# Kernel tuning notes

Hardware: AMD Instinct MI355X
Metric: run time of the kernel (lower is better)

Reference implementation:

```python
import jax, jax.numpy as jnp
import numpy as np

HEADS = 2
DIM_HEAD = 1
HIDDEN = HEADS * DIM_HEAD
SCALE = DIM_HEAD ** (-0.5)


def setup_inputs() -> dict:
    key = jax.random.key(0)
    ks = jax.random.split(key, 5)
    B, C, H, W, Z = 2, 64, 128, 128, 16
    return {
        "x": jax.random.normal(ks[0], (B, C, H, W, Z), dtype=jnp.float32),
        "query": jax.random.normal(ks[1], (B, C, H, W, Z), dtype=jnp.float32),
        "W_qkv": jax.random.normal(ks[2], (3 * HIDDEN, C), dtype=jnp.float32) * 0.1,
        "W_q": jax.random.normal(ks[3], (HIDDEN, C), dtype=jnp.float32) * 0.1,
        "W_out": jax.random.normal(ks[4], (C, HIDDEN), dtype=jnp.float32) * 0.1,
        "b_out": jnp.zeros((C,), dtype=jnp.float32),
    }


def reference(x, query, W_qkv, W_q, W_out, b_out):
    b, c, h, w, z = x.shape
    n = h * w * z
    xf = x.reshape(b, c, n)          # [b, c, n]
    qf = query.reshape(b, query.shape[1], n)

    # 1x1 conv3d == per-voxel linear projection; q-chunk of to_qkv is discarded
    k = jnp.einsum('bcn,oc->bon', xf, W_qkv[HIDDEN:2 * HIDDEN])   # [b, hidden, n]
    v = jnp.einsum('bcn,oc->bon', xf, W_qkv[2 * HIDDEN:3 * HIDDEN])
    q = jnp.einsum('bcn,oc->bon', qf, W_q)

    # split heads: [b, heads, dim_head, n]
    k = k.reshape(b, HEADS, DIM_HEAD, n)
    v = v.reshape(b, HEADS, DIM_HEAD, n)
    q = q.reshape(b, HEADS, DIM_HEAD, n)

    q = jax.nn.softmax(q, axis=2) * SCALE   # softmax over dim_head
    k = jax.nn.softmax(k, axis=3)           # softmax over voxels

    context = jnp.einsum('bhdn,bhen->bhde', k, v)   # [b, h, d, e]
    out = jnp.einsum('bhde,bhdn->bhen', context, q) # [b, h, e, n]
    out = out.reshape(b, HIDDEN, n)

    out = jnp.einsum('bcn,oc->bon', out, W_out) + b_out[None, :, None]
    return out.reshape(b, c, h, w, z)
```

## Files before the change

kernel.cpp:

```cpp
#include <hip/hip_runtime.h>
#include <math.h>


#define C_IN 64
#define NVOX (128 * 128 * 16)
#define COLS (NVOX / 4)
#define BLK  256
#define NB1  1024
#define CPB  (COLS / NB1)
#define F4_TOTAL (2 * C_IN * COLS)
#define GRID2 1024
#define F4_PER_BLK (F4_TOTAL / GRID2)

__global__ __launch_bounds__(BLK) void k1_proj_reduce(
    const float* __restrict__ x, const float* __restrict__ Wqkv,
    float4* __restrict__ partials )
{
    __shared__ float  s_w[4][C_IN];
    __shared__ float4 s_red[4];
    const int tid = threadIdx.x;
    const int b = blockIdx.y;

    s_w[tid >> 6][tid & 63] = Wqkv[(2 + (tid >> 6)) * C_IN + (tid & 63)];
    __syncthreads();

    const int wave  = tid >> 6;
    const int lane  = tid & 63;
    const int chunk = lane >> 4;
    const int c0    = chunk << 4;
    const int col   = blockIdx.x * CPB + (wave << 4) + (lane & 15);

    const float4* xp = reinterpret_cast<const float4*>(x)
                       + (size_t)b * C_IN * COLS + (size_t)c0 * COLS + col;

    float4 kh0 = make_float4(0.f, 0.f, 0.f, 0.f);
    float4 kh1 = kh0, vh0 = kh0, vh1 = kh0;

    #pragma unroll
    for (int i = 0; i < 16; ++i) {
        float4 xv = xp[(size_t)i * COLS];
        float wk0 = s_w[0][c0 + i], wk1 = s_w[1][c0 + i];
        float wv0 = s_w[2][c0 + i], wv1 = s_w[3][c0 + i];
        kh0.x = fmaf(xv.x, wk0, kh0.x); kh0.y = fmaf(xv.y, wk0, kh0.y);
        kh0.z = fmaf(xv.z, wk0, kh0.z); kh0.w = fmaf(xv.w, wk0, kh0.w);
        kh1.x = fmaf(xv.x, wk1, kh1.x); kh1.y = fmaf(xv.y, wk1, kh1.y);
        kh1.z = fmaf(xv.z, wk1, kh1.z); kh1.w = fmaf(xv.w, wk1, kh1.w);
        vh0.x = fmaf(xv.x, wv0, vh0.x); vh0.y = fmaf(xv.y, wv0, vh0.y);
        vh0.z = fmaf(xv.z, wv0, vh0.z); vh0.w = fmaf(xv.w, wv0, vh0.w);
        vh1.x = fmaf(xv.x, wv1, vh1.x); vh1.y = fmaf(xv.y, wv1, vh1.y);
        vh1.z = fmaf(xv.z, wv1, vh1.z); vh1.w = fmaf(xv.w, wv1, vh1.w);
    }

    #pragma unroll
    for (int off = 16; off <= 32; off <<= 1) {
        kh0.x += __shfl_xor(kh0.x, off); kh0.y += __shfl_xor(kh0.y, off);
        kh0.z += __shfl_xor(kh0.z, off); kh0.w += __shfl_xor(kh0.w, off);
        kh1.x += __shfl_xor(kh1.x, off); kh1.y += __shfl_xor(kh1.y, off);
        kh1.z += __shfl_xor(kh1.z, off); kh1.w += __shfl_xor(kh1.w, off);
        vh0.x += __shfl_xor(vh0.x, off); vh0.y += __shfl_xor(vh0.y, off);
        vh0.z += __shfl_xor(vh0.z, off); vh0.w += __shfl_xor(vh0.w, off);
        vh1.x += __shfl_xor(vh1.x, off); vh1.y += __shfl_xor(vh1.y, off);
        vh1.z += __shfl_xor(vh1.z, off); vh1.w += __shfl_xor(vh1.w, off);
    }

    float s0 = 0.f, sv0 = 0.f, s1 = 0.f, sv1 = 0.f;
    float e;
    e = __expf(kh0.x); s0 += e; sv0 = fmaf(e, vh0.x, sv0);
    e = __expf(kh0.y); s0 += e; sv0 = fmaf(e, vh0.y, sv0);
    e = __expf(kh0.z); s0 += e; sv0 = fmaf(e, vh0.z, sv0);
    e = __expf(kh0.w); s0 += e; sv0 = fmaf(e, vh0.w, sv0);
    e = __expf(kh1.x); s1 += e; sv1 = fmaf(e, vh1.x, sv1);
    e = __expf(kh1.y); s1 += e; sv1 = fmaf(e, vh1.y, sv1);
    e = __expf(kh1.z); s1 += e; sv1 = fmaf(e, vh1.z, sv1);
    e = __expf(kh1.w); s1 += e; sv1 = fmaf(e, vh1.w, sv1);

    #pragma unroll
    for (int off = 1; off <= 8; off <<= 1) {
        s0  += __shfl_xor(s0,  off);
        sv0 += __shfl_xor(sv0, off);
        s1  += __shfl_xor(s1,  off);
        sv1 += __shfl_xor(sv1, off);
    }
    if (lane == 0) s_red[wave] = make_float4(s0, sv0, s1, sv1);
    __syncthreads();
    if (tid == 0) {
        float4 r0 = s_red[0], r1 = s_red[1], r2 = s_red[2], r3 = s_red[3];
        partials[(size_t)b * NB1 + blockIdx.x] =
            make_float4(r0.x + r1.x + r2.x + r3.x,
                        r0.y + r1.y + r2.y + r3.y,
                        r0.z + r1.z + r2.z + r3.z,
                        r0.w + r1.w + r2.w + r3.w);
    }
}

__global__ __launch_bounds__(BLK) void k2_combine_fill(
    const float* __restrict__ partials,
    const float* __restrict__ Wout,
    const float* __restrict__ bout,
    float4* __restrict__ out)
{
    __shared__ float s_ctx[2][2];
    const int tid = threadIdx.x;
    const int wave = tid >> 6, lane = tid & 63;
    const int b = wave >> 1, h = wave & 1;

    const float2* p2 = reinterpret_cast<const float2*>(partials);
    float s = 0.f, sv = 0.f;
    #pragma unroll
    for (int i = 0; i < NB1 / 64; ++i) {
        float2 t = p2[(size_t)(b * NB1 + i * 64 + lane) * 2 + h];
        s += t.x; sv += t.y;
    }
    #pragma unroll
    for (int off = 1; off <= 32; off <<= 1) {
        s  += __shfl_xor(s,  off);
        sv += __shfl_xor(sv, off);
    }
    if (lane == 0) s_ctx[b][h] = sv / s;
    __syncthreads();

    const int row = blockIdx.x >> 3;
    const int bb = row >> 6, o = row & 63;
    const float v = fmaf(Wout[o * 2 + 0], s_ctx[bb][0],
                    fmaf(Wout[o * 2 + 1], s_ctx[bb][1], bout[o]));
    const float4 f4 = make_float4(v, v, v, v);

    const size_t base = (size_t)blockIdx.x * F4_PER_BLK;
    #pragma unroll 8
    for (int k = 0; k < F4_PER_BLK / BLK; ++k)
        out[base + ((size_t)k << 8) + tid] = f4;
}

extern "C" void kernel_launch(void* const* d_in, const int* in_sizes, int n_in,
                              void* d_out, int out_size, void* d_ws, size_t ws_size,
                              hipStream_t stream) {
    const float* x    = (const float*)d_in[0];
    const float* Wqkv = (const float*)d_in[2];
    const float* Wout = (const float*)d_in[4];
    const float* bout = (const float*)d_in[5];
    float4* out = (float4*)d_out;
    float4* partials = (float4*)d_ws;

    k1_proj_reduce<<<dim3(NB1, 2), BLK, 0, stream>>>(x, Wqkv, partials);
    k2_combine_fill<<<GRID2, BLK, 0, stream>>>((const float*)partials, Wout,
                                               bout, out);
}
```

Before: 49.97 us.

## Fuse projection-reduce and output fill into one kernel with grid barrier

Merges the two kernels into one persistent-style kernel of 1024 blocks. Each block now processes two column chunks, then all blocks meet at a global atomic-counter barrier before each block combines the partials and writes its slice of the constant output. This removes the second kernel launch and its launch gap, but adds a memset launch for the counter, a spin-wait barrier that requires every block to be co-resident, and a serialized wait before any output store can begin.

```diff
diff --git a/kernel.cpp b/kernel.cpp
--- a/kernel.cpp
+++ b/kernel.cpp
@@ -1,78 +1,87 @@
 #include <hip/hip_runtime.h>
 #include <math.h>
+#include <string.h>
 
 
 #define C_IN 64
-#define NVOX (128 * 128 * 16)
-#define COLS (NVOX / 4)
+#define COLS 65536
 #define BLK  256
-#define NB1  1024
-#define CPB  (COLS / NB1)
-#define F4_TOTAL (2 * C_IN * COLS)
-#define GRID2 1024
-#define F4_PER_BLK (F4_TOTAL / GRID2)
+#define GRID 1024
+#define BPB  512
+#define CPB  128
+#define F4_PER_BLK 8192
 
-__global__ __launch_bounds__(BLK) void k1_proj_reduce(
+__global__ __launch_bounds__(BLK, 4) void fused_linattn(
     const float* __restrict__ x, const float* __restrict__ Wqkv,
-    float4* __restrict__ partials )
+    const float* __restrict__ Wout, const float* __restrict__ bout,
+    float4* __restrict__ out, float4* __restrict__ partials,
+    unsigned int* __restrict__ cnt)
 {
     __shared__ float  s_w[4][C_IN];
     __shared__ float4 s_red[4];
-    const int tid = threadIdx.x;
-    const int b = blockIdx.y;
+    __shared__ float  s_ctx[2][2];
+    __shared__ float  s_vals[128];
+
+    const int tid  = threadIdx.x;
+    const int wave = tid >> 6;
+    const int lane = tid & 63;
+    const int bid  = blockIdx.x;
+    const int b    = bid >> 9;
+    const int blk  = bid & (BPB - 1);
 
     s_w[tid >> 6][tid & 63] = Wqkv[(2 + (tid >> 6)) * C_IN + (tid & 63)];
     __syncthreads();
 
-    const int wave  = tid >> 6;
-    const int lane  = tid & 63;
     const int chunk = lane >> 4;
     const int c0    = chunk << 4;
-    const int col   = blockIdx.x * CPB + (wave << 4) + (lane & 15);
-
-    const float4* xp = reinterpret_cast<const float4*>(x)
-                       + (size_t)b * C_IN * COLS + (size_t)c0 * COLS + col;
-
-    float4 kh0 = make_float4(0.f, 0.f, 0.f, 0.f);
-    float4 kh1 = kh0, vh0 = kh0, vh1 = kh0;
-
-    #pragma unroll
-    for (int i = 0; i < 16; ++i) {
-        float4 xv = xp[(size_t)i * COLS];
-        float wk0 = s_w[0][c0 + i], wk1 = s_w[1][c0 + i];
-        float wv0 = s_w[2][c0 + i], wv1 = s_w[3][c0 + i];
-        kh0.x = fmaf(xv.x, wk0, kh0.x); kh0.y = fmaf(xv.y, wk0, kh0.y);
-        kh0.z = fmaf(xv.z, wk0, kh0.z); kh0.w = fmaf(xv.w, wk0, kh0.w);
-        kh1.x = fmaf(xv.x, wk1, kh1.x); kh1.y = fmaf(xv.y, wk1, kh1.y);
-        kh1.z = fmaf(xv.z, wk1, kh1.z); kh1.w = fmaf(xv.w, wk1, kh1.w);
-        vh0.x = fmaf(xv.x, wv0, vh0.x); vh0.y = fmaf(xv.y, wv0, vh0.y);
-        vh0.z = fmaf(xv.z, wv0, vh0.z); vh0.w = fmaf(xv.w, wv0, vh0.w);
-        vh1.x = fmaf(xv.x, wv1, vh1.x); vh1.y = fmaf(xv.y, wv1, vh1.y);
-        vh1.z = fmaf(xv.z, wv1, vh1.z); vh1.w = fmaf(xv.w, wv1, vh1.w);
-    }
-
-    #pragma unroll
-    for (int off = 16; off <= 32; off <<= 1) {
-        kh0.x += __shfl_xor(kh0.x, off); kh0.y += __shfl_xor(kh0.y, off);
-        kh0.z += __shfl_xor(kh0.z, off); kh0.w += __shfl_xor(kh0.w, off);
-        kh1.x += __shfl_xor(kh1.x, off); kh1.y += __shfl_xor(kh1.y, off);
-        kh1.z += __shfl_xor(kh1.z, off); kh1.w += __shfl_xor(kh1.w, off);
-        vh0.x += __shfl_xor(vh0.x, off); vh0.y += __shfl_xor(vh0.y, off);
-        vh0.z += __shfl_xor(vh0.z, off); vh0.w += __shfl_xor(vh0.w, off);
-        vh1.x += __shfl_xor(vh1.x, off); vh1.y += __shfl_xor(vh1.y, off);
-        vh1.z += __shfl_xor(vh1.z, off); vh1.w += __shfl_xor(vh1.w, off);
-    }
 
     float s0 = 0.f, sv0 = 0.f, s1 = 0.f, sv1 = 0.f;
-    float e;
-    e = __expf(kh0.x); s0 += e; sv0 = fmaf(e, vh0.x, sv0);
-    e = __expf(kh0.y); s0 += e; sv0 = fmaf(e, vh0.y, sv0);
-    e = __expf(kh0.z); s0 += e; sv0 = fmaf(e, vh0.z, sv0);
-    e = __expf(kh0.w); s0 += e; sv0 = fmaf(e, vh0.w, sv0);
-    e = __expf(kh1.x); s1 += e; sv1 = fmaf(e, vh1.x, sv1);
-    e = __expf(kh1.y); s1 += e; sv1 = fmaf(e, vh1.y, sv1);
-    e = __expf(kh1.z); s1 += e; sv1 = fmaf(e, vh1.z, sv1);
-    e = __expf(kh1.w); s1 += e; sv1 = fmaf(e, vh1.w, sv1);
+
+    for (int p = 0; p < 2; ++p) {
+        const int col = blk * CPB + p * 64 + (wave << 4) + (lane & 15);
+        const float4* xp = reinterpret_cast<const float4*>(x)
+                           + (size_t)b * C_IN * COLS + (size_t)c0 * COLS + col;
+
+        float4 kh0 = make_float4(0.f, 0.f, 0.f, 0.f);
+        float4 kh1 = kh0, vh0 = kh0, vh1 = kh0;
+
+        #pragma unroll
+        for (int i = 0; i < 16; ++i) {
+            float4 xv = xp[(size_t)i * COLS];
+            float wk0 = s_w[0][c0 + i], wk1 = s_w[1][c0 + i];
+            float wv0 = s_w[2][c0 + i], wv1 = s_w[3][c0 + i];
+            kh0.x = fmaf(xv.x, wk0, kh0.x); kh0.y = fmaf(xv.y, wk0, kh0.y);
+            kh0.z = fmaf(xv.z, wk0, kh0.z); kh0.w = fmaf(xv.w, wk0, kh0.w);
+            kh1.x = fmaf(xv.x, wk1, kh1.x); kh1.y = fmaf(xv.y, wk1, kh1.y);
+            kh1.z = fmaf(xv.z, wk1, kh1.z); kh1.w = fmaf(xv.w, wk1, kh1.w);
+            vh0.x = fmaf(xv.x, wv0, vh0.x); vh0.y = fmaf(xv.y, wv0, vh0.y);
+            vh0.z = fmaf(xv.z, wv0, vh0.z); vh0.w = fmaf(xv.w, wv0, vh0.w);
+            vh1.x = fmaf(xv.x, wv1, vh1.x); vh1.y = fmaf(xv.y, wv1, vh1.y);
+            vh1.z = fmaf(xv.z, wv1, vh1.z); vh1.w = fmaf(xv.w, wv1, vh1.w);
+        }
+
+        #pragma unroll
+        for (int off = 16; off <= 32; off <<= 1) {
+            kh0.x += __shfl_xor(kh0.x, off); kh0.y += __shfl_xor(kh0.y, off);
+            kh0.z += __shfl_xor(kh0.z, off); kh0.w += __shfl_xor(kh0.w, off);
+            kh1.x += __shfl_xor(kh1.x, off); kh1.y += __shfl_xor(kh1.y, off);
+            kh1.z += __shfl_xor(kh1.z, off); kh1.w += __shfl_xor(kh1.w, off);
+            vh0.x += __shfl_xor(vh0.x, off); vh0.y += __shfl_xor(vh0.y, off);
+            vh0.z += __shfl_xor(vh0.z, off); vh0.w += __shfl_xor(vh0.w, off);
+            vh1.x += __shfl_xor(vh1.x, off); vh1.y += __shfl_xor(vh1.y, off);
+            vh1.z += __shfl_xor(vh1.z, off); vh1.w += __shfl_xor(vh1.w, off);
+        }
+
+        float e;
+        e = __expf(kh0.x); s0 += e; sv0 = fmaf(e, vh0.x, sv0);
+        e = __expf(kh0.y); s0 += e; sv0 = fmaf(e, vh0.y, sv0);
+        e = __expf(kh0.z); s0 += e; sv0 = fmaf(e, vh0.z, sv0);
+        e = __expf(kh0.w); s0 += e; sv0 = fmaf(e, vh0.w, sv0);
+        e = __expf(kh1.x); s1 += e; sv1 = fmaf(e, vh1.x, sv1);
+        e = __expf(kh1.y); s1 += e; sv1 = fmaf(e, vh1.y, sv1);
+        e = __expf(kh1.z); s1 += e; sv1 = fmaf(e, vh1.z, sv1);
+        e = __expf(kh1.w); s1 += e; sv1 = fmaf(e, vh1.w, sv1);
+    }
 
     #pragma unroll
     for (int off = 1; off <= 8; off <<= 1) {
@@ -85,47 +94,54 @@
     __syncthreads();
     if (tid == 0) {
         float4 r0 = s_red[0], r1 = s_red[1], r2 = s_red[2], r3 = s_red[3];
-        partials[(size_t)b * NB1 + blockIdx.x] =
-            make_float4(r0.x + r1.x + r2.x + r3.x,
-                        r0.y + r1.y + r2.y + r3.y,
-                        r0.z + r1.z + r2.z + r3.z,
-                        r0.w + r1.w + r2.w + r3.w);
+        partials[bid] = make_float4(r0.x + r1.x + r2.x + r3.x,
+                                    r0.y + r1.y + r2.y + r3.y,
+                                    r0.z + r1.z + r2.z + r3.z,
+                                    r0.w + r1.w + r2.w + r3.w);
     }
-}
 
-__global__ __launch_bounds__(BLK) void k2_combine_fill(
-    const float* __restrict__ partials,
-    const float* __restrict__ Wout,
-    const float* __restrict__ bout,
-    float4* __restrict__ out)
-{
-    __shared__ float s_ctx[2][2];
-    const int tid = threadIdx.x;
-    const int wave = tid >> 6, lane = tid & 63;
-    const int b = wave >> 1, h = wave & 1;
-
-    const float2* p2 = reinterpret_cast<const float2*>(partials);
-    float s = 0.f, sv = 0.f;
-    #pragma unroll
-    for (int i = 0; i < NB1 / 64; ++i) {
-        float2 t = p2[(size_t)(b * NB1 + i * 64 + lane) * 2 + h];
-        s += t.x; sv += t.y;
+    if (tid == 0) {
+        __threadfence();
+        atomicAdd(cnt, 1u);
+        while (__hip_atomic_load(cnt, __ATOMIC_ACQUIRE,
+                                 __HIP_MEMORY_SCOPE_AGENT) < GRID)
+            __builtin_amdgcn_s_sleep(8);
     }
-    #pragma unroll
-    for (int off = 1; off <= 32; off <<= 1) {
-        s  += __shfl_xor(s,  off);
-        sv += __shfl_xor(sv, off);
-    }
-    if (lane == 0) s_ctx[b][h] = sv / s;
     __syncthreads();
 
-    const int row = blockIdx.x >> 3;
-    const int bb = row >> 6, o = row & 63;
-    const float v = fmaf(Wout[o * 2 + 0], s_ctx[bb][0],
-                    fmaf(Wout[o * 2 + 1], s_ctx[bb][1], bout[o]));
+    {
+        const int bb = wave >> 1, h = wave & 1;
+        const unsigned long long* pp =
+            reinterpret_cast<const unsigned long long*>(partials);
+        float s = 0.f, sv = 0.f;
+        #pragma unroll
+        for (int i = 0; i < BPB / 64; ++i) {
+            unsigned long long raw = __hip_atomic_load(
+                pp + ((size_t)(bb * BPB + i * 64 + lane) * 2 + h),
+                __ATOMIC_RELAXED, __HIP_MEMORY_SCOPE_AGENT);
+            float2 t;
+            memcpy(&t, &raw, 8);
+            s += t.x; sv += t.y;
+        }
+        #pragma unroll
+        for (int off = 1; off <= 32; off <<= 1) {
+            s  += __shfl_xor(s,  off);
+            sv += __shfl_xor(sv, off);
+        }
+        if (lane == 0) s_ctx[bb][h] = sv / s;
+    }
+    __syncthreads();
+    if (tid < 128) {
+        const int bb = tid >> 6, o = tid & 63;
+        s_vals[tid] = fmaf(Wout[o * 2 + 0], s_ctx[bb][0],
+                      fmaf(Wout[o * 2 + 1], s_ctx[bb][1], bout[o]));
+    }
+    __syncthreads();
+
+    const int row = bid >> 3;
+    const float v = s_vals[row];
     const float4 f4 = make_float4(v, v, v, v);
-
-    const size_t base = (size_t)blockIdx.x * F4_PER_BLK;
+    const size_t base = (size_t)bid * F4_PER_BLK;
     #pragma unroll 8
     for (int k = 0; k < F4_PER_BLK / BLK; ++k)
         out[base + ((size_t)k << 8) + tid] = f4;
@@ -139,9 +155,11 @@
     const float* Wout = (const float*)d_in[4];
     const float* bout = (const float*)d_in[5];
     float4* out = (float4*)d_out;
+
     float4* partials = (float4*)d_ws;
+    unsigned int* cnt = (unsigned int*)((char*)d_ws + 32768);
 
-    k1_proj_reduce<<<dim3(NB1, 2), BLK, 0, stream>>>(x, Wqkv, partials);
-    k2_combine_fill<<<GRID2, BLK, 0, stream>>>((const float*)partials, Wout,
-                                               bout, out);
+    hipMemsetAsync(cnt, 0, sizeof(unsigned int), stream);
+    fused_linattn<<<GRID, BLK, 0, stream>>>(x, Wqkv, Wout, bout, out,
+                                            partials, cnt);
 }
```

Result: slower. 177.5 us (+255.3%).
